# Performance work log

Hardware: AMD Instinct MI355X
Metric: run time of the kernel (lower is better)

## Reference

```python
import jax, jax.numpy as jnp
import numpy as np

N_NODES, FEAT, EMB, BATCH, NUM_SAMPLE = 100000, 256, 256, 10000, 32


def setup_inputs() -> dict:
    key = jax.random.key(0)
    ks = jax.random.split(key, 8)
    sc = 1.0 / np.sqrt(FEAT).astype(np.float32)
    return {
        "nodes": jax.random.randint(ks[0], (BATCH,), 0, N_NODES),
        "neigh_idx": jax.random.randint(ks[1], (BATCH, NUM_SAMPLE), 0, N_NODES),
        "id2feat": jax.random.normal(ks[2], (N_NODES, FEAT), jnp.float32),
        "Wq": jax.random.normal(ks[3], (FEAT, EMB), jnp.float32) * sc,
        "bq": jnp.zeros((EMB,), jnp.float32),
        "Wk": jax.random.normal(ks[4], (FEAT, EMB), jnp.float32) * sc,
        "bk": jnp.zeros((EMB,), jnp.float32),
        "Wv": jax.random.normal(ks[5], (FEAT, EMB), jnp.float32) * sc,
        "bv": jnp.zeros((EMB,), jnp.float32),
    }


def reference(nodes, neigh_idx, id2feat, Wq, bq, Wk, bk, Wv, bv):
    # Gather: self feats [B, F] and sampled neighbor feats [B, S, F]
    self_feats = id2feat[nodes]
    neigh_feats = id2feat[neigh_idx]
    S = neigh_idx.shape[1]
    # Keys/values over [neighbors, self] -> [B, S+1, F]
    cat = jnp.concatenate([neigh_feats, self_feats[:, None, :]], axis=1)
    Q = self_feats @ Wq + bq               # [B, E]
    K = cat @ Wk + bk                       # [B, S+1, E]
    V = cat @ Wv + bv                       # [B, S+1, E]
    scores = jnp.einsum('be,bse->bs', Q, K)  # [B, S+1]
    # Faithful to original mask loop: with full neighbor lists, columns >= num_sample
    # (the appended self key) are masked out.
    mask = jnp.arange(S + 1) >= S
    scores = jnp.where(mask[None, :], -jnp.inf, scores)
    attn = jax.nn.softmax(scores, axis=-1)   # [B, S+1]
    return jnp.einsum('bs,bse->be', attn, V)  # [B, E]
```

## Files before the change

kernel.cpp:

```cpp
#include <hip/hip_runtime.h>
#include <math.h>

#define F 256
#define E 256
#define S 32
#define CH 4

typedef __attribute__((ext_vector_type(8))) short short8;
typedef __attribute__((ext_vector_type(4))) float f32x4;

__device__ __forceinline__ ushort f2bf(float x) {
    uint u = __float_as_uint(x);
    return (ushort)((u + 0x7fffu + ((u >> 16) & 1u)) >> 16);
}
__device__ __forceinline__ float bf2f(ushort h) {
    return __uint_as_float(((uint)h) << 16);
}
__device__ __forceinline__ uint4 pack8(const ushort* h) {
    uint4 r;
    r.x = (uint)h[0] | ((uint)h[1] << 16); r.y = (uint)h[2] | ((uint)h[3] << 16);
    r.z = (uint)h[4] | ((uint)h[5] << 16); r.w = (uint)h[6] | ((uint)h[7] << 16);
    return r;
}
__device__ __forceinline__ void split4(const float* x, uint2& ph, uint2& pl) {
    ushort h[4], l[4];
#pragma unroll
    for (int i = 0; i < 4; ++i) { h[i] = f2bf(x[i]); l[i] = f2bf(x[i] - bf2f(h[i])); }
    ph.x = (uint)h[0] | ((uint)h[1] << 16); ph.y = (uint)h[2] | ((uint)h[3] << 16);
    pl.x = (uint)l[0] | ((uint)l[1] << 16); pl.y = (uint)l[2] | ((uint)l[3] << 16);
}
__device__ __forceinline__ void split8(const float* x, short8& h, short8& l) {
    ushort hh[8], ll[8];
#pragma unroll
    for (int i = 0; i < 8; ++i) { hh[i] = f2bf(x[i]); ll[i] = f2bf(x[i] - bf2f(hh[i])); }
    uint4 ph = pack8(hh), pl = pack8(ll);
    h = *reinterpret_cast<short8*>(&ph);
    l = *reinterpret_cast<short8*>(&pl);
}
__device__ __forceinline__ short8 mk8(uint a, uint b, uint c, uint d) {
    uint4 p = make_uint4(a, b, c, d);
    return *reinterpret_cast<short8*>(&p);
}
__device__ __forceinline__ uint pkbf(float v) {
    const ushort h = f2bf(v);
    const ushort l = f2bf(v - bf2f(h));
    return (uint)h | ((uint)l << 16);
}

__global__ __launch_bounds__(512) void prep(const float* __restrict__ Wq,
                                            const float* __restrict__ bq,
                                            const float* __restrict__ Wk,
                                            const float* __restrict__ Wv,
                                            ushort* __restrict__ MTh,
                                            ushort* __restrict__ MTl,
                                            ushort* __restrict__ WvTh,
                                            ushort* __restrict__ WvTl,
                                            float* __restrict__ c) {
    const int blk = blockIdx.x, tid = threadIdx.x;
    const int lane = tid & 63, wave = tid >> 6;
    if (blk < 4) {
        const int wm = wave >> 2, wn = wave & 3;
        const int fr = lane & 15, fk = lane >> 4;
        const int j0 = blk * 64;
        f32x4 acc[2][4];
#pragma unroll
        for (int m = 0; m < 2; ++m)
#pragma unroll
            for (int n = 0; n < 4; ++n) acc[m][n] = (f32x4){0.f, 0.f, 0.f, 0.f};
        for (int k0 = 0; k0 < F; k0 += 32) {
            short8 ah[2], al[2];
#pragma unroll
            for (int m = 0; m < 2; ++m) {
                const float* p = &Wk[(size_t)(j0 + wm * 32 + m * 16 + fr) * F + k0 + fk * 8];
                float x[8];
                *reinterpret_cast<float4*>(&x[0]) = *reinterpret_cast<const float4*>(p);
                *reinterpret_cast<float4*>(&x[4]) = *reinterpret_cast<const float4*>(p + 4);
                split8(x, ah[m], al[m]);
            }
#pragma unroll
            for (int n = 0; n < 4; ++n) {
                const float* p = &Wq[(size_t)(wn * 64 + n * 16 + fr) * F + k0 + fk * 8];
                float x[8];
                *reinterpret_cast<float4*>(&x[0]) = *reinterpret_cast<const float4*>(p);
                *reinterpret_cast<float4*>(&x[4]) = *reinterpret_cast<const float4*>(p + 4);
                short8 bh, bl;
                split8(x, bh, bl);
#pragma unroll
                for (int m = 0; m < 2; ++m) {
                    acc[m][n] = __builtin_amdgcn_mfma_f32_16x16x32_bf16(ah[m], bh, acc[m][n], 0, 0, 0);
                    acc[m][n] = __builtin_amdgcn_mfma_f32_16x16x32_bf16(ah[m], bl, acc[m][n], 0, 0, 0);
                    acc[m][n] = __builtin_amdgcn_mfma_f32_16x16x32_bf16(al[m], bh, acc[m][n], 0, 0, 0);
                }
            }
        }
#pragma unroll
        for (int n = 0; n < 4; ++n) {
            const int i = wn * 64 + n * 16 + fr;
#pragma unroll
            for (int m = 0; m < 2; ++m)
#pragma unroll
                for (int r = 0; r < 4; ++r) {
                    const int j = j0 + wm * 32 + m * 16 + fk * 4 + r;
                    const float v = acc[m][n][r];
                    const ushort h = f2bf(v);
                    MTh[(size_t)j * F + i] = h;
                    MTl[(size_t)j * F + i] = f2bf(v - bf2f(h));
                }
        }
    } else if (blk < 20) {
        __shared__ float t[64][65];
        const int tb = blk - 4;
        const int jt = (tb & 3) * 64, kt = (tb >> 2) * 64;
        const int lk = tid >> 3, lj = (tid & 7) * 8;
        {
            const float* p = &Wv[(size_t)(kt + lk) * E + jt + lj];
            const float4 v0 = *reinterpret_cast<const float4*>(p);
            const float4 v1 = *reinterpret_cast<const float4*>(p + 4);
            t[lk][lj + 0] = v0.x; t[lk][lj + 1] = v0.y; t[lk][lj + 2] = v0.z; t[lk][lj + 3] = v0.w;
            t[lk][lj + 4] = v1.x; t[lk][lj + 5] = v1.y; t[lk][lj + 6] = v1.z; t[lk][lj + 7] = v1.w;
        }
        __syncthreads();
        const int oj = tid >> 3, ok = (tid & 7) * 8;
        ushort h[8], l[8];
#pragma unroll
        for (int u = 0; u < 8; ++u) {
            const float v = t[ok + u][oj];
            h[u] = f2bf(v); l[u] = f2bf(v - bf2f(h[u]));
        }
        *reinterpret_cast<uint4*>(&WvTh[(size_t)(jt + oj) * F + kt + ok]) = pack8(h);
        *reinterpret_cast<uint4*>(&WvTl[(size_t)(jt + oj) * F + kt + ok]) = pack8(l);
    } else {
        __shared__ float bqs[F];
        if (tid < F) bqs[tid] = bq[tid];
        __syncthreads();
        const float4 b4 = *reinterpret_cast<const float4*>(&bqs[lane * 4]);
#pragma unroll
        for (int i = 0; i < 8; ++i) {
            const int j = (blk - 20) * 64 + wave * 8 + i;
            const float4 k4 = *reinterpret_cast<const float4*>(&Wk[(size_t)j * F + lane * 4]);
            float p = k4.x * b4.x + k4.y * b4.y + k4.z * b4.z + k4.w * b4.w;
#pragma unroll
            for (int off = 32; off; off >>= 1) p += __shfl_xor(p, off);
            if (lane == 0) c[j] = p;
        }
    }
}

__global__ __launch_bounds__(256) void qgemm(const float* __restrict__ X,
                                             const int* __restrict__ nodes,
                                             const ushort* __restrict__ BTh,
                                             const ushort* __restrict__ BTl,
                                             const float* __restrict__ cb,
                                             float* __restrict__ outq,
                                             int B) {
    __shared__ ushort Ah[2][32][40], Al[2][32][40];
    const int tid = threadIdx.x, lane = tid & 63, wave = tid >> 6;
    const int fr = lane & 15, fk = lane >> 4;
    const int row0 = blockIdx.x * 32;
    const int col0 = blockIdx.y * 128 + wave * 32;

    const int arL = tid >> 3, akL = (tid & 7) * 4;
    const int gr = row0 + arL;
    const int grc = gr < B ? gr : B - 1;
    const float* aptr = X + (size_t)nodes[grc] * F + akL;

    f32x4 acc[2][2];
#pragma unroll
    for (int m = 0; m < 2; ++m)
#pragma unroll
        for (int n = 0; n < 2; ++n) acc[m][n] = (f32x4){0.f, 0.f, 0.f, 0.f};

    {
        const float4 av = *reinterpret_cast<const float4*>(aptr);
        uint2 h, l; split4(&av.x, h, l);
        *reinterpret_cast<uint2*>(&Ah[0][arL][akL]) = h;
        *reinterpret_cast<uint2*>(&Al[0][arL][akL]) = l;
    }
    __syncthreads();

    for (int t = 0; t < 8; ++t) {
        const int cur = t & 1;
        float4 nv;
        if (t < 7) nv = *reinterpret_cast<const float4*>(aptr + (t + 1) * 32);

        short8 a_h[2], a_l[2];
#pragma unroll
        for (int m = 0; m < 2; ++m) {
            a_h[m] = *reinterpret_cast<const short8*>(&Ah[cur][m * 16 + fr][fk * 8]);
            a_l[m] = *reinterpret_cast<const short8*>(&Al[cur][m * 16 + fr][fk * 8]);
        }
#pragma unroll
        for (int n = 0; n < 2; ++n) {
            const size_t boff = (size_t)(col0 + n * 16 + fr) * F + t * 32 + fk * 8;
            const short8 bh = *reinterpret_cast<const short8*>(&BTh[boff]);
            const short8 bl = *reinterpret_cast<const short8*>(&BTl[boff]);
#pragma unroll
            for (int m = 0; m < 2; ++m) {
                acc[m][n] = __builtin_amdgcn_mfma_f32_16x16x32_bf16(a_h[m], bh, acc[m][n], 0, 0, 0);
                acc[m][n] = __builtin_amdgcn_mfma_f32_16x16x32_bf16(a_h[m], bl, acc[m][n], 0, 0, 0);
                acc[m][n] = __builtin_amdgcn_mfma_f32_16x16x32_bf16(a_l[m], bh, acc[m][n], 0, 0, 0);
            }
        }
        if (t < 7) {
            uint2 h, l; split4(&nv.x, h, l);
            *reinterpret_cast<uint2*>(&Ah[cur ^ 1][arL][akL]) = h;
            *reinterpret_cast<uint2*>(&Al[cur ^ 1][arL][akL]) = l;
        }
        __syncthreads();
    }

#pragma unroll
    for (int n = 0; n < 2; ++n) {
        const int col = col0 + n * 16 + fr;
        const float cc = cb[col];
#pragma unroll
        for (int m = 0; m < 2; ++m)
#pragma unroll
            for (int r = 0; r < 4; ++r) {
                const int row = row0 + m * 16 + fk * 4 + r;
                if (row < B) outq[(size_t)row * F + col] = acc[m][n][r] + cc;
            }
    }
}

__device__ __forceinline__ void ld_chunk(float4* d, int idxv, int s0,
                                         const float* __restrict__ t, int lane) {
#pragma unroll
    for (int j = 0; j < CH; ++j) {
        const int nid = __builtin_amdgcn_readlane(idxv, s0 + j);
        d[j] = *reinterpret_cast<const float4*>(&t[(size_t)nid * F + lane * 4]);
    }
}
__device__ __forceinline__ void proc_chunk(const float4* v, const float4 qv,
                                           float& m, float& l, float4& acc) {
#pragma unroll
    for (int j = 0; j < CH; ++j) {
        float p = v[j].x * qv.x + v[j].y * qv.y + v[j].z * qv.z + v[j].w * qv.w;
#pragma unroll
        for (int off = 32; off; off >>= 1) p += __shfl_xor(p, off);
        if (p <= m) {
            const float w = __expf(p - m);
            l += w;
            acc.x += w * v[j].x; acc.y += w * v[j].y;
            acc.z += w * v[j].z; acc.w += w * v[j].w;
        } else {
            const float cc = __expf(m - p);
            l = l * cc + 1.f;
            acc.x = acc.x * cc + v[j].x; acc.y = acc.y * cc + v[j].y;
            acc.z = acc.z * cc + v[j].z; acc.w = acc.w * cc + v[j].w;
            m = p;
        }
    }
}

__global__ __launch_bounds__(256) void gatherD(const int* __restrict__ neigh,
                                               const float* __restrict__ id2feat,
                                               const float* __restrict__ qtm,
                                               const ushort* __restrict__ WvTh,
                                               const float* __restrict__ bv,
                                               float* __restrict__ out,
                                               int B) {
    __shared__ uint tile[4][260];
    const int tid = threadIdx.x, lane = tid & 63, wave = tid >> 6;
    const int node = blockIdx.x * 4 + wave;

    if (node < B) {
        const int idxv = neigh[node * S + (lane & (S - 1))];
        const float4 qv = *reinterpret_cast<const float4*>(&qtm[(size_t)node * F + lane * 4]);
        float m = -INFINITY, l = 0.f;
        float4 a = make_float4(0.f, 0.f, 0.f, 0.f);
        float4 va[CH], vb[CH];
        ld_chunk(va, idxv, 0, id2feat, lane);
        ld_chunk(vb, idxv, 4, id2feat, lane);
        proc_chunk(va, qv, m, l, a);
        ld_chunk(va, idxv, 8, id2feat, lane);
        proc_chunk(vb, qv, m, l, a);
        ld_chunk(vb, idxv, 12, id2feat, lane);
        proc_chunk(va, qv, m, l, a);
        ld_chunk(va, idxv, 16, id2feat, lane);
        proc_chunk(vb, qv, m, l, a);
        ld_chunk(vb, idxv, 20, id2feat, lane);
        proc_chunk(va, qv, m, l, a);
        ld_chunk(va, idxv, 24, id2feat, lane);
        proc_chunk(vb, qv, m, l, a);
        ld_chunk(vb, idxv, 28, id2feat, lane);
        proc_chunk(va, qv, m, l, a);
        proc_chunk(vb, qv, m, l, a);
        const float inv = 1.0f / l;
        const uint4 o = make_uint4(pkbf(a.x * inv), pkbf(a.y * inv),
                                   pkbf(a.z * inv), pkbf(a.w * inv));
        *reinterpret_cast<uint4*>(&tile[wave][lane * 4]) = o;
    }
    __syncthreads();

    const int fr = lane & 15, fk = lane >> 4;
    f32x4 acc[4];
#pragma unroll
    for (int n = 0; n < 4; ++n) acc[n] = (f32x4){0.f, 0.f, 0.f, 0.f};

    for (int k0 = 0; k0 < F; k0 += 32) {
        const uint4 u0 = *reinterpret_cast<const uint4*>(&tile[fr & 3][k0 + fk * 8]);
        const uint4 u1 = *reinterpret_cast<const uint4*>(&tile[fr & 3][k0 + fk * 8 + 4]);
        const short8 ah = mk8((u0.x & 0xffffu) | (u0.y << 16), (u0.z & 0xffffu) | (u0.w << 16),
                              (u1.x & 0xffffu) | (u1.y << 16), (u1.z & 0xffffu) | (u1.w << 16));
        const short8 al = mk8((u0.x >> 16) | (u0.y & 0xffff0000u), (u0.z >> 16) | (u0.w & 0xffff0000u),
                              (u1.x >> 16) | (u1.y & 0xffff0000u), (u1.z >> 16) | (u1.w & 0xffff0000u));
#pragma unroll
        for (int n = 0; n < 4; ++n) {
            const size_t boff = (size_t)(wave * 64 + n * 16 + fr) * F + k0 + fk * 8;
            const short8 bh = *reinterpret_cast<const short8*>(&WvTh[boff]);
            acc[n] = __builtin_amdgcn_mfma_f32_16x16x32_bf16(ah, bh, acc[n], 0, 0, 0);
            acc[n] = __builtin_amdgcn_mfma_f32_16x16x32_bf16(al, bh, acc[n], 0, 0, 0);
        }
    }
    if (fk == 0) {
#pragma unroll
        for (int n = 0; n < 4; ++n) {
            const int col = wave * 64 + n * 16 + fr;
            const float bb = bv[col];
#pragma unroll
            for (int r = 0; r < 4; ++r) {
                const int grow = blockIdx.x * 4 + r;
                if (grow < B) out[(size_t)grow * E + col] = acc[n][r] + bb;
            }
        }
    }
}

extern "C" void kernel_launch(void* const* d_in, const int* in_sizes, int n_in,
                              void* d_out, int out_size, void* d_ws, size_t ws_size,
                              hipStream_t stream) {
    const int*   nodes   = (const int*)d_in[0];
    const int*   neigh   = (const int*)d_in[1];
    const float* id2feat = (const float*)d_in[2];
    const float* Wq      = (const float*)d_in[3];
    const float* bq      = (const float*)d_in[4];
    const float* Wk      = (const float*)d_in[5];
    const float* Wv      = (const float*)d_in[7];
    const float* bv      = (const float*)d_in[8];
    float* out = (float*)d_out;
    const int B = in_sizes[0];

    ushort* MTh  = (ushort*)d_ws;
    ushort* MTl  = MTh + 65536;
    ushort* WvTh = MTl + 65536;
    ushort* WvTl = WvTh + 65536;
    float*  cbuf = (float*)(WvTl + 65536);
    float*  qtm  = cbuf + 256;

    prep<<<dim3(24), dim3(512), 0, stream>>>(Wq, bq, Wk, Wv, MTh, MTl, WvTh, WvTl, cbuf);
    qgemm<<<dim3((B + 31) / 32, 2), dim3(256), 0, stream>>>(id2feat, nodes,
                                                            MTh, MTl, cbuf, qtm, B);
    gatherD<<<dim3((B + 3) / 4), dim3(256), 0, stream>>>(neigh, id2feat, qtm,
                                                         WvTh, bv, out, B);
}
```

Baseline: 123.5 us.

## Split attention gather from Wv projection into separate GEMM kernel

The fused gather kernel, which did the attention-weighted neighbour sum and then a 4-row MFMA projection with Wv, is split in two. The gather kernel now writes the fp32 aggregated features in place over the Q buffer. A generic 32-row GEMM kernel, reused from the Q projection, then applies Wv with bias, using the 3-term bf16 split (hi/lo) instead of 2 terms. This aims to avoid the poor Wv reuse of 4-row tiles, at the cost of an extra launch and an extra round trip of the intermediate through global memory.

```diff
diff --git a/kernel.cpp b/kernel.cpp
--- a/kernel.cpp
+++ b/kernel.cpp
@@ -36,15 +36,6 @@
     uint4 ph = pack8(hh), pl = pack8(ll);
     h = *reinterpret_cast<short8*>(&ph);
     l = *reinterpret_cast<short8*>(&pl);
-}
-__device__ __forceinline__ short8 mk8(uint a, uint b, uint c, uint d) {
-    uint4 p = make_uint4(a, b, c, d);
-    return *reinterpret_cast<short8*>(&p);
-}
-__device__ __forceinline__ uint pkbf(float v) {
-    const ushort h = f2bf(v);
-    const ushort l = f2bf(v - bf2f(h));
-    return (uint)h | ((uint)l << 16);
 }
 
 __global__ __launch_bounds__(512) void prep(const float* __restrict__ Wq,
@@ -146,13 +137,13 @@
     }
 }
 
-__global__ __launch_bounds__(256) void qgemm(const float* __restrict__ X,
-                                             const int* __restrict__ nodes,
-                                             const ushort* __restrict__ BTh,
-                                             const ushort* __restrict__ BTl,
-                                             const float* __restrict__ cb,
-                                             float* __restrict__ outq,
-                                             int B) {
+__global__ __launch_bounds__(256) void gemm32(const float* __restrict__ X,
+                                              const int* __restrict__ idx,
+                                              const ushort* __restrict__ BTh,
+                                              const ushort* __restrict__ BTl,
+                                              const float* __restrict__ bias,
+                                              float* __restrict__ outp,
+                                              int rows) {
     __shared__ ushort Ah[2][32][40], Al[2][32][40];
     const int tid = threadIdx.x, lane = tid & 63, wave = tid >> 6;
     const int fr = lane & 15, fk = lane >> 4;
@@ -161,8 +152,9 @@
 
     const int arL = tid >> 3, akL = (tid & 7) * 4;
     const int gr = row0 + arL;
-    const int grc = gr < B ? gr : B - 1;
-    const float* aptr = X + (size_t)nodes[grc] * F + akL;
+    const int grc = gr < rows ? gr : rows - 1;
+    const long arow = idx ? (long)idx[grc] : (long)grc;
+    const float* aptr = X + arow * (long)F + akL;
 
     f32x4 acc[2][2];
 #pragma unroll
@@ -212,13 +204,13 @@
 #pragma unroll
     for (int n = 0; n < 2; ++n) {
         const int col = col0 + n * 16 + fr;
-        const float cc = cb[col];
+        const float cc = bias[col];
 #pragma unroll
         for (int m = 0; m < 2; ++m)
 #pragma unroll
             for (int r = 0; r < 4; ++r) {
                 const int row = row0 + m * 16 + fk * 4 + r;
-                if (row < B) outq[(size_t)row * F + col] = acc[m][n][r] + cc;
+                if (row < rows) outp[(size_t)row * F + col] = acc[m][n][r] + cc;
             }
     }
 }
@@ -253,78 +245,42 @@
     }
 }
 
-__global__ __launch_bounds__(256) void gatherD(const int* __restrict__ neigh,
-                                               const float* __restrict__ id2feat,
-                                               const float* __restrict__ qtm,
-                                               const ushort* __restrict__ WvTh,
-                                               const float* __restrict__ bv,
-                                               float* __restrict__ out,
-                                               int B) {
-    __shared__ uint tile[4][260];
-    const int tid = threadIdx.x, lane = tid & 63, wave = tid >> 6;
-    const int node = blockIdx.x * 4 + wave;
-
-    if (node < B) {
-        const int idxv = neigh[node * S + (lane & (S - 1))];
-        const float4 qv = *reinterpret_cast<const float4*>(&qtm[(size_t)node * F + lane * 4]);
-        float m = -INFINITY, l = 0.f;
-        float4 a = make_float4(0.f, 0.f, 0.f, 0.f);
-        float4 va[CH], vb[CH];
-        ld_chunk(va, idxv, 0, id2feat, lane);
-        ld_chunk(vb, idxv, 4, id2feat, lane);
-        proc_chunk(va, qv, m, l, a);
-        ld_chunk(va, idxv, 8, id2feat, lane);
-        proc_chunk(vb, qv, m, l, a);
-        ld_chunk(vb, idxv, 12, id2feat, lane);
-        proc_chunk(va, qv, m, l, a);
-        ld_chunk(va, idxv, 16, id2feat, lane);
-        proc_chunk(vb, qv, m, l, a);
-        ld_chunk(vb, idxv, 20, id2feat, lane);
-        proc_chunk(va, qv, m, l, a);
-        ld_chunk(va, idxv, 24, id2feat, lane);
-        proc_chunk(vb, qv, m, l, a);
-        ld_chunk(vb, idxv, 28, id2feat, lane);
-        proc_chunk(va, qv, m, l, a);
-        proc_chunk(vb, qv, m, l, a);
-        const float inv = 1.0f / l;
-        const uint4 o = make_uint4(pkbf(a.x * inv), pkbf(a.y * inv),
-                                   pkbf(a.z * inv), pkbf(a.w * inv));
-        *reinterpret_cast<uint4*>(&tile[wave][lane * 4]) = o;
-    }
-    __syncthreads();
-
-    const int fr = lane & 15, fk = lane >> 4;
-    f32x4 acc[4];
-#pragma unroll
-    for (int n = 0; n < 4; ++n) acc[n] = (f32x4){0.f, 0.f, 0.f, 0.f};
-
-    for (int k0 = 0; k0 < F; k0 += 32) {
-        const uint4 u0 = *reinterpret_cast<const uint4*>(&tile[fr & 3][k0 + fk * 8]);
-        const uint4 u1 = *reinterpret_cast<const uint4*>(&tile[fr & 3][k0 + fk * 8 + 4]);
-        const short8 ah = mk8((u0.x & 0xffffu) | (u0.y << 16), (u0.z & 0xffffu) | (u0.w << 16),
-                              (u1.x & 0xffffu) | (u1.y << 16), (u1.z & 0xffffu) | (u1.w << 16));
-        const short8 al = mk8((u0.x >> 16) | (u0.y & 0xffff0000u), (u0.z >> 16) | (u0.w & 0xffff0000u),
-                              (u1.x >> 16) | (u1.y & 0xffff0000u), (u1.z >> 16) | (u1.w & 0xffff0000u));
-#pragma unroll
-        for (int n = 0; n < 4; ++n) {
-            const size_t boff = (size_t)(wave * 64 + n * 16 + fr) * F + k0 + fk * 8;
-            const short8 bh = *reinterpret_cast<const short8*>(&WvTh[boff]);
-            acc[n] = __builtin_amdgcn_mfma_f32_16x16x32_bf16(ah, bh, acc[n], 0, 0, 0);
-            acc[n] = __builtin_amdgcn_mfma_f32_16x16x32_bf16(al, bh, acc[n], 0, 0, 0);
-        }
-    }
-    if (fk == 0) {
-#pragma unroll
-        for (int n = 0; n < 4; ++n) {
-            const int col = wave * 64 + n * 16 + fr;
-            const float bb = bv[col];
-#pragma unroll
-            for (int r = 0; r < 4; ++r) {
-                const int grow = blockIdx.x * 4 + r;
-                if (grow < B) out[(size_t)grow * E + col] = acc[n][r] + bb;
-            }
-        }
-    }
+__global__ __launch_bounds__(256) void attn_gather(const int* __restrict__ neigh_idx,
+                                                   const float* __restrict__ id2feat,
+                                                   float* __restrict__ qtm,
+                                                   int B) {
+    const int node = blockIdx.x * 4 + (threadIdx.x >> 6);
+    const int lane = threadIdx.x & 63;
+    if (node >= B) return;
+
+    const int idxv = neigh_idx[node * S + (lane & (S - 1))];
+    const float4 qv = *reinterpret_cast<const float4*>(&qtm[(size_t)node * F + lane * 4]);
+
+    float m = -INFINITY, l = 0.f;
+    float4 acc = make_float4(0.f, 0.f, 0.f, 0.f);
+
+    float4 va[CH], vb[CH];
+    ld_chunk(va, idxv, 0, id2feat, lane);
+    ld_chunk(vb, idxv, 4, id2feat, lane);
+    proc_chunk(va, qv, m, l, acc);
+    ld_chunk(va, idxv, 8, id2feat, lane);
+    proc_chunk(vb, qv, m, l, acc);
+    ld_chunk(vb, idxv, 12, id2feat, lane);
+    proc_chunk(va, qv, m, l, acc);
+    ld_chunk(va, idxv, 16, id2feat, lane);
+    proc_chunk(vb, qv, m, l, acc);
+    ld_chunk(vb, idxv, 20, id2feat, lane);
+    proc_chunk(va, qv, m, l, acc);
+    ld_chunk(va, idxv, 24, id2feat, lane);
+    proc_chunk(vb, qv, m, l, acc);
+    ld_chunk(vb, idxv, 28, id2feat, lane);
+    proc_chunk(va, qv, m, l, acc);
+    proc_chunk(vb, qv, m, l, acc);
+
+    const float inv = 1.0f / l;
+    float4 o;
+    o.x = acc.x * inv; o.y = acc.y * inv; o.z = acc.z * inv; o.w = acc.w * inv;
+    *reinterpret_cast<float4*>(&qtm[(size_t)node * F + lane * 4]) = o;
 }
 
 extern "C" void kernel_launch(void* const* d_in, const int* in_sizes, int n_in,
@@ -349,8 +305,9 @@
     float*  qtm  = cbuf + 256;
 
     prep<<<dim3(24), dim3(512), 0, stream>>>(Wq, bq, Wk, Wv, MTh, MTl, WvTh, WvTl, cbuf);
-    qgemm<<<dim3((B + 31) / 32, 2), dim3(256), 0, stream>>>(id2feat, nodes,
-                                                            MTh, MTl, cbuf, qtm, B);
-    gatherD<<<dim3((B + 3) / 4), dim3(256), 0, stream>>>(neigh, id2feat, qtm,
-                                                         WvTh, bv, out, B);
-}
+    gemm32<<<dim3((B + 31) / 32, 2), dim3(256), 0, stream>>>(id2feat, nodes,
+                                                             MTh, MTl, cbuf, qtm, B);
+    attn_gather<<<dim3((B + 3) / 4), dim3(256), 0, stream>>>(neigh, id2feat, qtm, B);
+    gemm32<<<dim3((B + 31) / 32, 2), dim3(256), 0, stream>>>(qtm, nullptr,
+                                                             WvTh, WvTl, bv, out, B);
+}
```

Result: faster. 120.2 us, median of 2 (-2.7%).
